# Kernel optimization log

Hardware: AMD Instinct MI355X
Metric: run time of the kernel (lower is better)

## Reference

```python
import jax, jax.numpy as jnp
import numpy as np

B, T, D = 4, 4096, 1024
P = 64  # d_model / n_head

def setup_inputs() -> dict:
    key = jax.random.key(0)
    k1, k2, k3 = jax.random.split(key, 3)
    x = jax.random.normal(k1, (B, T, D), dtype=jnp.float32)
    Wqkv = jax.random.normal(k2, (D, 3 * P), dtype=jnp.float32) * (1.0 / np.sqrt(D))
    bqkv = jax.random.normal(k3, (3 * P,), dtype=jnp.float32) * 0.01
    return {"x": x, "Wqkv": Wqkv, "bqkv": bqkv}

def reference(x, Wqkv, bqkv):
    Bv, Tv, Cv = x.shape
    qkv = (x @ Wqkv + bqkv).reshape(Bv, Tv, 3, P)  # [B,T,3,p]
    q, k, v = qkv[:, :, 0, :], qkv[:, :, 1, :], qkv[:, :, 2, :]
    # raw scores (source applies NO 1/sqrt(p) scaling)
    S = jnp.einsum('btp,bsp->bts', q, k)  # [B,T,T]
    causal = jnp.tril(jnp.ones((Tv, Tv), dtype=bool))
    S = jnp.where(causal[None, :, :], S, jnp.float32(-jnp.inf))
    Pm = jax.nn.softmax(S, axis=-1)
    O = jnp.einsum('bts,bsp->btp', Pm, v)  # [B,T,p]
    return O
```

## Files before the change

### kernel.cpp

```cpp
#include <hip/hip_runtime.h>
#include <hip/hip_fp16.h>

#define B_ 4
#define T_ 4096
#define D_ 1024
#define P_ 64

typedef _Float16 h8 __attribute__((ext_vector_type(8)));
typedef _Float16 h4 __attribute__((ext_vector_type(4)));
typedef float f32x4 __attribute__((ext_vector_type(4)));

__global__ __launch_bounds__(256) void wt_kernel(const float* __restrict__ W,
                                                 _Float16* __restrict__ Wt) {
    int idx = blockIdx.x * 256 + threadIdx.x;
    int n = idx >> 10, k = idx & 1023;
    Wt[idx] = (_Float16)W[k * 192 + n];
}

__global__ __launch_bounds__(256) void proj_kernel(
    const float* __restrict__ x, const _Float16* __restrict__ Wt,
    const float* __restrict__ bias,
    _Float16* __restrict__ qh, _Float16* __restrict__ kh, _Float16* __restrict__ vh)
{
    __shared__ _Float16 As[2][32][72];
    __shared__ _Float16 Bs[2][192][72];
    const int tid = threadIdx.x;
    const int w = tid >> 6, lane = tid & 63, quad = lane >> 4, l16 = lane & 15;
    const int row0 = blockIdx.x * 32;
    const int mstrip = w & 1;
    const int nbase = (w >> 1) * 6;

    float bvals[6];
#pragma unroll
    for (int nt = 0; nt < 6; nt++) bvals[nt] = bias[(nbase + nt) * 16 + l16];

    f32x4 acc[6];
#pragma unroll
    for (int i = 0; i < 6; i++) acc[i] = (f32x4){0.f, 0.f, 0.f, 0.f};

    const int arow = tid >> 3, ac0 = (tid & 7) * 8;

    float4 xa, xb;
    h8 wreg[6];
    {
        const float* xp = x + (size_t)(row0 + arow) * D_ + ac0;
        xa = *(const float4*)xp; xb = *(const float4*)(xp + 4);
#pragma unroll
        for (int p = 0; p < 6; p++) {
            int f = tid + 256 * p; int n = f >> 3, c0 = (f & 7) * 8;
            wreg[p] = *(const h8*)(Wt + (size_t)n * D_ + c0);
        }
    }

    for (int kc = 0; kc < 16; kc++) {
        const int buf = kc & 1;
        h8 av;
        av[0]=(_Float16)xa.x; av[1]=(_Float16)xa.y; av[2]=(_Float16)xa.z; av[3]=(_Float16)xa.w;
        av[4]=(_Float16)xb.x; av[5]=(_Float16)xb.y; av[6]=(_Float16)xb.z; av[7]=(_Float16)xb.w;
        *(h8*)&As[buf][arow][ac0] = av;
#pragma unroll
        for (int p = 0; p < 6; p++) {
            int f = tid + 256 * p; int n = f >> 3, c0 = (f & 7) * 8;
            *(h8*)&Bs[buf][n][c0] = wreg[p];
        }
        if (kc + 1 < 16) {
            int k0 = (kc + 1) * 64;
            const float* xp = x + (size_t)(row0 + arow) * D_ + k0 + ac0;
            xa = *(const float4*)xp; xb = *(const float4*)(xp + 4);
#pragma unroll
            for (int p = 0; p < 6; p++) {
                int f = tid + 256 * p; int n = f >> 3, c0 = (f & 7) * 8;
                wreg[p] = *(const h8*)(Wt + (size_t)n * D_ + k0 + c0);
            }
        }
        __syncthreads();
        h8 a0 = *(const h8*)&As[buf][16 * mstrip + l16][quad * 8];
        h8 a1 = *(const h8*)&As[buf][16 * mstrip + l16][32 + quad * 8];
#pragma unroll
        for (int nt = 0; nt < 6; nt++) {
            h8 b0 = *(const h8*)&Bs[buf][(nbase + nt) * 16 + l16][quad * 8];
            h8 b1 = *(const h8*)&Bs[buf][(nbase + nt) * 16 + l16][32 + quad * 8];
            acc[nt] = __builtin_amdgcn_mfma_f32_16x16x32_f16(a0, b0, acc[nt], 0, 0, 0);
            acc[nt] = __builtin_amdgcn_mfma_f32_16x16x32_f16(a1, b1, acc[nt], 0, 0, 0);
        }
    }

#pragma unroll
    for (int nt = 0; nt < 6; nt++) {
        int n = (nbase + nt) * 16 + l16;
        int g = n >> 6, p = n & 63;
        _Float16* dst = (g == 0) ? qh : (g == 1) ? kh : vh;
#pragma unroll
        for (int reg = 0; reg < 4; reg++) {
            int trow = row0 + 16 * mstrip + quad * 4 + reg;
            dst[(size_t)trow * 64 + p] = (_Float16)(acc[nt][reg] + bvals[nt]);
        }
    }
}

__global__ __launch_bounds__(256) void attn_kernel(
    const _Float16* __restrict__ qh, const _Float16* __restrict__ kh,
    const _Float16* __restrict__ vh, float* __restrict__ out,
    float* __restrict__ Opart, float2* __restrict__ ml,
    int lgC, int NC1, int direct)
{
    __shared__ _Float16 Vt[2][80][72];
    __shared__ _Float16 Ps[4][16][72];
    const int tid = threadIdx.x;
    const int w = tid >> 6, lane = tid & 63, quad = lane >> 4, l16 = lane & 15;
    const int C = 1 << lgC;

    const int cid = blockIdx.x;
    const int b = cid / NC1;
    int rem = cid - b * NC1;
    int qt = 0, k0 = 0, cnt = 1;
    for (int q = 0; q < 64; q++) {
        int nc = (q + C) >> lgC;
        if (rem < nc) { qt = q; k0 = rem << lgC; cnt = min(C, q + 1 - k0); break; }
        rem -= nc;
    }
    const size_t base = (size_t)b * T_ * 64;

#pragma unroll
    for (int buf = 0; buf < 2; buf++)
#pragma unroll
        for (int i = 0; i < 4; i++) {
            int r = 64 + i * 4 + w;
            Vt[buf][r][lane] = (r == 64) ? (_Float16)1.0f : (_Float16)0.0f;
        }

    h8 qf[2];
    {
        const _Float16* qp = qh + base + (size_t)(qt * 64 + 16 * w + l16) * 64 + quad * 8;
        qf[0] = *(const h8*)qp;
        qf[1] = *(const h8*)(qp + 32);
    }

    f32x4 o[5];
#pragma unroll
    for (int i = 0; i < 5; i++) o[i] = (f32x4){0.f, 0.f, 0.f, 0.f};
    float m[4];
#pragma unroll
    for (int r = 0; r < 4; r++) m[r] = -1e30f;

    const int vp0 = (tid & 15) * 4, vc0 = (tid >> 4) * 4;
    h4 vreg[4];
    {
        const _Float16* vp = vh + base + (size_t)(k0 * 64 + vc0) * 64 + vp0;
#pragma unroll
        for (int i = 0; i < 4; i++) vreg[i] = *(const h4*)(vp + (size_t)i * 64);
    }

    const int kend = k0 + cnt;
    for (int kt = k0; kt < kend; kt++) {
        const int bufi = kt & 1;
        h8 kf[4][2];
        {
            const _Float16* kp = kh + base + (size_t)(kt * 64 + l16) * 64 + quad * 8;
#pragma unroll
            for (int nt = 0; nt < 4; nt++) {
                kf[nt][0] = *(const h8*)(kp + (size_t)nt * 16 * 64);
                kf[nt][1] = *(const h8*)(kp + (size_t)nt * 16 * 64 + 32);
            }
        }
#pragma unroll
        for (int j = 0; j < 4; j++) {
            h4 t;
            t[0] = vreg[0][j]; t[1] = vreg[1][j]; t[2] = vreg[2][j]; t[3] = vreg[3][j];
            *(h4*)&Vt[bufi][vp0 + j][vc0] = t;
        }
        if (kt + 1 < kend) {
            const _Float16* vp = vh + base + (size_t)((kt + 1) * 64 + vc0) * 64 + vp0;
#pragma unroll
            for (int i = 0; i < 4; i++) vreg[i] = *(const h4*)(vp + (size_t)i * 64);
        }
        __syncthreads();

        f32x4 s[4];
#pragma unroll
        for (int nt = 0; nt < 4; nt++) {
            f32x4 c = (f32x4){0.f, 0.f, 0.f, 0.f};
            c = __builtin_amdgcn_mfma_f32_16x16x32_f16(qf[0], kf[nt][0], c, 0, 0, 0);
            c = __builtin_amdgcn_mfma_f32_16x16x32_f16(qf[1], kf[nt][1], c, 0, 0, 0);
            s[nt] = c;
        }

        if (kt == qt) {
#pragma unroll
            for (int nt = 0; nt < 4; nt++)
#pragma unroll
                for (int reg = 0; reg < 4; reg++) {
                    int col = nt * 16 + l16, row = 16 * w + quad * 4 + reg;
                    if (col > row) s[nt][reg] = -1e30f;
                }
        }

        float pexp[4][4];
#pragma unroll
        for (int reg = 0; reg < 4; reg++) {
            float mx = fmaxf(fmaxf(s[0][reg], s[1][reg]), fmaxf(s[2][reg], s[3][reg]));
            mx = fmaxf(mx, __shfl_xor(mx, 1));
            mx = fmaxf(mx, __shfl_xor(mx, 2));
            mx = fmaxf(mx, __shfl_xor(mx, 4));
            mx = fmaxf(mx, __shfl_xor(mx, 8));
            float mnew = fmaxf(m[reg], mx);
            float alpha = __expf(m[reg] - mnew);
            m[reg] = mnew;
#pragma unroll
            for (int nt = 0; nt < 4; nt++) pexp[nt][reg] = __expf(s[nt][reg] - mnew);
#pragma unroll
            for (int nt = 0; nt < 5; nt++) o[nt][reg] *= alpha;
        }

#pragma unroll
        for (int nt = 0; nt < 4; nt++)
#pragma unroll
            for (int reg = 0; reg < 4; reg++)
                Ps[w][quad * 4 + reg][nt * 16 + l16] = (_Float16)pexp[nt][reg];

#pragma unroll
        for (int kc = 0; kc < 2; kc++) {
            h8 pa = *(const h8*)&Ps[w][l16][kc * 32 + quad * 8];
#pragma unroll
            for (int nt = 0; nt < 5; nt++) {
                h8 vb = *(const h8*)&Vt[bufi][nt * 16 + l16][kc * 32 + quad * 8];
                o[nt] = __builtin_amdgcn_mfma_f32_16x16x32_f16(pa, vb, o[nt], 0, 0, 0);
            }
        }
    }

    if (direct) {
        float linv[4];
#pragma unroll
        for (int reg = 0; reg < 4; reg++) {
            float lv = __shfl(o[4][reg], quad << 4);
            linv[reg] = 1.0f / lv;
        }
#pragma unroll
        for (int nt = 0; nt < 4; nt++)
#pragma unroll
            for (int reg = 0; reg < 4; reg++) {
                int trow = qt * 64 + 16 * w + quad * 4 + reg;
                out[base + (size_t)trow * 64 + nt * 16 + l16] = o[nt][reg] * linv[reg];
            }
    } else {
        float* op = Opart + (size_t)cid * 4096;
#pragma unroll
        for (int nt = 0; nt < 4; nt++)
#pragma unroll
            for (int reg = 0; reg < 4; reg++)
                op[(16 * w + quad * 4 + reg) * 64 + nt * 16 + l16] = o[nt][reg];
        if (l16 == 0) {
#pragma unroll
            for (int reg = 0; reg < 4; reg++) {
                int r = 16 * w + quad * 4 + reg;
                ml[(size_t)cid * 64 + r] = make_float2(m[reg], o[4][reg]);
            }
        }
    }
}

__global__ __launch_bounds__(256) void combine_kernel(
    const float* __restrict__ Opart, const float2* __restrict__ ml,
    float* __restrict__ out, int lgC, int NC1)
{
    const int C = 1 << lgC;
    const int task = blockIdx.x;
    const int b = task >> 6, qt = task & 63;
    int pref = 0;
    for (int q = 0; q < qt; q++) pref += (q + C) >> lgC;
    const int cbase = b * NC1 + pref;
    const int nch = (qt + C) >> lgC;

    const int r = threadIdx.x >> 2;
    const int c0 = (threadIdx.x & 3) << 4;

    float M = -1e30f;
    for (int i = 0; i < nch; i++) M = fmaxf(M, ml[(size_t)(cbase + i) * 64 + r].x);
    float L = 0.f, acc[16];
#pragma unroll
    for (int t = 0; t < 16; t++) acc[t] = 0.f;
    for (int i = 0; i < nch; i++) {
        float2 v = ml[(size_t)(cbase + i) * 64 + r];
        float sc = __expf(v.x - M);
        L += sc * v.y;
        const float* op = Opart + (size_t)(cbase + i) * 4096 + r * 64 + c0;
#pragma unroll
        for (int t = 0; t < 4; t++) {
            float4 x4 = *(const float4*)(op + 4 * t);
            acc[4*t+0] += sc * x4.x; acc[4*t+1] += sc * x4.y;
            acc[4*t+2] += sc * x4.z; acc[4*t+3] += sc * x4.w;
        }
    }
    float inv = 1.0f / L;
    float* po = out + ((size_t)b * T_ + qt * 64 + r) * 64 + c0;
#pragma unroll
    for (int t = 0; t < 4; t++) {
        float4 x4 = { acc[4*t]*inv, acc[4*t+1]*inv, acc[4*t+2]*inv, acc[4*t+3]*inv };
        *(float4*)(po + 4 * t) = x4;
    }
}

extern "C" void kernel_launch(void* const* d_in, const int* in_sizes, int n_in,
                              void* d_out, int out_size, void* d_ws, size_t ws_size,
                              hipStream_t stream) {
    const float* x    = (const float*)d_in[0];
    const float* W    = (const float*)d_in[1];
    const float* bias = (const float*)d_in[2];
    float* out = (float*)d_out;
    char* ws = (char*)d_ws;
    _Float16* qh = (_Float16*)(ws);
    _Float16* kh = (_Float16*)(ws + (size_t)2 * 1024 * 1024);
    _Float16* vh = (_Float16*)(ws + (size_t)4 * 1024 * 1024);
    _Float16* Wt = (_Float16*)(ws + (size_t)6 * 1024 * 1024);
    const size_t pbase = (size_t)8 * 1024 * 1024;

    int lgC = -1, nc1 = 64;
    for (int lg = 3; lg <= 6; lg++) {
        int C = 1 << lg, n1 = 0;
        for (int q = 0; q < 64; q++) n1 += (q + C) >> lg;
        size_t need = pbase + (size_t)4 * n1 * (4096 * 4 + 64 * 8);
        if (need <= ws_size) { lgC = lg; nc1 = n1; break; }
    }
    int direct = (lgC < 0) ? 1 : 0;
    if (direct) { lgC = 6; nc1 = 64; }
    float*  Opart = (float*)(ws + pbase);
    float2* mlp   = (float2*)(ws + pbase + (size_t)4 * nc1 * 4096 * 4);

    wt_kernel<<<768, 256, 0, stream>>>(W, Wt);
    proj_kernel<<<512, 256, 0, stream>>>(x, Wt, bias, qh, kh, vh);
    attn_kernel<<<4 * nc1, 256, 0, stream>>>(qh, kh, vh, out, Opart, mlp, lgC, nc1, direct);
    if (!direct)
        combine_kernel<<<256, 256, 0, stream>>>(Opart, mlp, out, lgC, nc1);
}
```

Baseline: 175.7 us.

## Rework attention to 128-row query tiles with LDS-staged K and exp2 softmax

Each attention block now covers 128 query rows, with 32 rows per wave. K tiles are staged through double-buffered LDS. Scores are computed transposed, so P stays in registers and feeds the PV MFMAs directly with no LDS round trip. Q is prescaled by log2e so the softmax can use exp2, and the row sum l is tracked explicitly instead of through an augmented ones column in V. Partial outputs are stored in fp16, the chunk size search now starts lower, and the W transpose and projection kernels are retiled (the projection splits N across two blocks). Together these aim to cut LDS traffic and redundant K loads. The cost is more registers per thread, occupancy now set through launch bounds, and slightly lower precision in the partial outputs.

New measurement: 176.2 us. No clear change (+0.3%).

```diff
diff --git a/kernel.cpp b/kernel.cpp
--- a/kernel.cpp
+++ b/kernel.cpp
@@ -4,17 +4,37 @@
 #define B_ 4
 #define T_ 4096
 #define D_ 1024
-#define P_ 64
 
 typedef _Float16 h8 __attribute__((ext_vector_type(8)));
 typedef _Float16 h4 __attribute__((ext_vector_type(4)));
 typedef float f32x4 __attribute__((ext_vector_type(4)));
 
+#define LOG2E 1.44269504088896340736f
+#define MASKV -3.0e38f
+#define MINIT -1.0e30f
+#define EXP2(x) __builtin_amdgcn_exp2f(x)
+
 __global__ __launch_bounds__(256) void wt_kernel(const float* __restrict__ W,
                                                  _Float16* __restrict__ Wt) {
-    int idx = blockIdx.x * 256 + threadIdx.x;
-    int n = idx >> 10, k = idx & 1023;
-    Wt[idx] = (_Float16)W[k * 192 + n];
+    __shared__ _Float16 Tr[192][20];
+    const int tid = threadIdx.x, k0 = blockIdx.x * 16;
+#pragma unroll
+    for (int i = 0; i < 3; i++) {
+        int fi = tid + 256 * i;
+        int r = fi / 48, c4 = fi % 48;
+        float4 v = *(const float4*)(W + (size_t)(k0 + r) * 192 + c4 * 4);
+        Tr[c4 * 4 + 0][r] = (_Float16)v.x;
+        Tr[c4 * 4 + 1][r] = (_Float16)v.y;
+        Tr[c4 * 4 + 2][r] = (_Float16)v.z;
+        Tr[c4 * 4 + 3][r] = (_Float16)v.w;
+    }
+    __syncthreads();
+#pragma unroll
+    for (int i = 0; i < 3; i++) {
+        int oi = tid + 256 * i;
+        int n = oi >> 2, kq = oi & 3;
+        *(h4*)(Wt + (size_t)n * D_ + k0 + kq * 4) = *(const h4*)&Tr[n][kq * 4];
+    }
 }
 
 __global__ __launch_bounds__(256) void proj_kernel(
@@ -23,32 +43,33 @@
     _Float16* __restrict__ qh, _Float16* __restrict__ kh, _Float16* __restrict__ vh)
 {
     __shared__ _Float16 As[2][32][72];
-    __shared__ _Float16 Bs[2][192][72];
+    __shared__ _Float16 Bs[2][96][72];
     const int tid = threadIdx.x;
     const int w = tid >> 6, lane = tid & 63, quad = lane >> 4, l16 = lane & 15;
-    const int row0 = blockIdx.x * 32;
+    const int row0 = (blockIdx.x >> 1) * 32;
+    const int nb0 = (blockIdx.x & 1) * 96;
     const int mstrip = w & 1;
-    const int nbase = (w >> 1) * 6;
-
-    float bvals[6];
-#pragma unroll
-    for (int nt = 0; nt < 6; nt++) bvals[nt] = bias[(nbase + nt) * 16 + l16];
-
-    f32x4 acc[6];
-#pragma unroll
-    for (int i = 0; i < 6; i++) acc[i] = (f32x4){0.f, 0.f, 0.f, 0.f};
+    const int ngrp = (w >> 1) * 3;
+
+    float bvals[3];
+#pragma unroll
+    for (int nt = 0; nt < 3; nt++) bvals[nt] = bias[nb0 + (ngrp + nt) * 16 + l16];
+
+    f32x4 acc[3];
+#pragma unroll
+    for (int i = 0; i < 3; i++) acc[i] = (f32x4){0.f, 0.f, 0.f, 0.f};
 
     const int arow = tid >> 3, ac0 = (tid & 7) * 8;
 
     float4 xa, xb;
-    h8 wreg[6];
+    h8 wreg[3];
     {
         const float* xp = x + (size_t)(row0 + arow) * D_ + ac0;
         xa = *(const float4*)xp; xb = *(const float4*)(xp + 4);
 #pragma unroll
-        for (int p = 0; p < 6; p++) {
+        for (int p = 0; p < 3; p++) {
             int f = tid + 256 * p; int n = f >> 3, c0 = (f & 7) * 8;
-            wreg[p] = *(const h8*)(Wt + (size_t)n * D_ + c0);
+            wreg[p] = *(const h8*)(Wt + (size_t)(nb0 + n) * D_ + c0);
         }
     }
 
@@ -59,7 +80,7 @@
         av[4]=(_Float16)xb.x; av[5]=(_Float16)xb.y; av[6]=(_Float16)xb.z; av[7]=(_Float16)xb.w;
         *(h8*)&As[buf][arow][ac0] = av;
 #pragma unroll
-        for (int p = 0; p < 6; p++) {
+        for (int p = 0; p < 3; p++) {
             int f = tid + 256 * p; int n = f >> 3, c0 = (f & 7) * 8;
             *(h8*)&Bs[buf][n][c0] = wreg[p];
         }
@@ -68,44 +89,45 @@
             const float* xp = x + (size_t)(row0 + arow) * D_ + k0 + ac0;
             xa = *(const float4*)xp; xb = *(const float4*)(xp + 4);
 #pragma unroll
-            for (int p = 0; p < 6; p++) {
+            for (int p = 0; p < 3; p++) {
                 int f = tid + 256 * p; int n = f >> 3, c0 = (f & 7) * 8;
-                wreg[p] = *(const h8*)(Wt + (size_t)n * D_ + k0 + c0);
+                wreg[p] = *(const h8*)(Wt + (size_t)(nb0 + n) * D_ + k0 + c0);
             }
         }
         __syncthreads();
         h8 a0 = *(const h8*)&As[buf][16 * mstrip + l16][quad * 8];
         h8 a1 = *(const h8*)&As[buf][16 * mstrip + l16][32 + quad * 8];
 #pragma unroll
-        for (int nt = 0; nt < 6; nt++) {
-            h8 b0 = *(const h8*)&Bs[buf][(nbase + nt) * 16 + l16][quad * 8];
-            h8 b1 = *(const h8*)&Bs[buf][(nbase + nt) * 16 + l16][32 + quad * 8];
+        for (int nt = 0; nt < 3; nt++) {
+            h8 b0 = *(const h8*)&Bs[buf][(ngrp + nt) * 16 + l16][quad * 8];
+            h8 b1 = *(const h8*)&Bs[buf][(ngrp + nt) * 16 + l16][32 + quad * 8];
             acc[nt] = __builtin_amdgcn_mfma_f32_16x16x32_f16(a0, b0, acc[nt], 0, 0, 0);
             acc[nt] = __builtin_amdgcn_mfma_f32_16x16x32_f16(a1, b1, acc[nt], 0, 0, 0);
         }
     }
 
 #pragma unroll
-    for (int nt = 0; nt < 6; nt++) {
-        int n = (nbase + nt) * 16 + l16;
+    for (int nt = 0; nt < 3; nt++) {
+        int n = nb0 + (ngrp + nt) * 16 + l16;
         int g = n >> 6, p = n & 63;
         _Float16* dst = (g == 0) ? qh : (g == 1) ? kh : vh;
+        float scale = (g == 0) ? LOG2E : 1.0f;
 #pragma unroll
         for (int reg = 0; reg < 4; reg++) {
             int trow = row0 + 16 * mstrip + quad * 4 + reg;
-            dst[(size_t)trow * 64 + p] = (_Float16)(acc[nt][reg] + bvals[nt]);
-        }
-    }
-}
-
-__global__ __launch_bounds__(256) void attn_kernel(
+            dst[(size_t)trow * 64 + p] = (_Float16)((acc[nt][reg] + bvals[nt]) * scale);
+        }
+    }
+}
+
+__global__ __launch_bounds__(256, 4) void attn_kernel(
     const _Float16* __restrict__ qh, const _Float16* __restrict__ kh,
     const _Float16* __restrict__ vh, float* __restrict__ out,
-    float* __restrict__ Opart, float2* __restrict__ ml,
+    _Float16* __restrict__ Opart, float2* __restrict__ ml,
     int lgC, int NC1, int direct)
 {
-    __shared__ _Float16 Vt[2][80][72];
-    __shared__ _Float16 Ps[4][16][72];
+    __shared__ _Float16 Ks[2][64][72];
+    __shared__ _Float16 Vt[2][64][72];
     const int tid = threadIdx.x;
     const int w = tid >> 6, lane = tid & 63, quad = lane >> 4, l16 = lane & 15;
     const int C = 1 << lgC;
@@ -113,39 +135,36 @@
     const int cid = blockIdx.x;
     const int b = cid / NC1;
     int rem = cid - b * NC1;
-    int qt = 0, k0 = 0, cnt = 1;
-    for (int q = 0; q < 64; q++) {
-        int nc = (q + C) >> lgC;
-        if (rem < nc) { qt = q; k0 = rem << lgC; cnt = min(C, q + 1 - k0); break; }
+    int qt2 = 0, k0 = 0, cnt = 1;
+    for (int i = 0; i < 32; i++) {
+        int nc = (2 * i + 2 + C - 1) >> lgC;
+        if (rem < nc) { qt2 = i; k0 = rem << lgC; cnt = min(C, 2 * i + 2 - k0); break; }
         rem -= nc;
     }
     const size_t base = (size_t)b * T_ * 64;
-
-#pragma unroll
-    for (int buf = 0; buf < 2; buf++)
-#pragma unroll
-        for (int i = 0; i < 4; i++) {
-            int r = 64 + i * 4 + w;
-            Vt[buf][r][lane] = (r == 64) ? (_Float16)1.0f : (_Float16)0.0f;
-        }
-
-    h8 qf[2];
-    {
-        const _Float16* qp = qh + base + (size_t)(qt * 64 + 16 * w + l16) * 64 + quad * 8;
-        qf[0] = *(const h8*)qp;
-        qf[1] = *(const h8*)(qp + 32);
-    }
-
-    f32x4 o[5];
-#pragma unroll
-    for (int i = 0; i < 5; i++) o[i] = (f32x4){0.f, 0.f, 0.f, 0.f};
-    float m[4];
-#pragma unroll
-    for (int r = 0; r < 4; r++) m[r] = -1e30f;
-
+    const int qbase = qt2 * 128 + w * 32;
+
+    h8 qf[2][2];
+#pragma unroll
+    for (int u = 0; u < 2; u++) {
+        const _Float16* qp = qh + base + (size_t)(qbase + u * 16 + l16) * 64 + quad * 8;
+        qf[u][0] = *(const h8*)qp;
+        qf[u][1] = *(const h8*)(qp + 32);
+    }
+
+    f32x4 o[8];
+#pragma unroll
+    for (int i = 0; i < 8; i++) o[i] = (f32x4){0.f, 0.f, 0.f, 0.f};
+    float m[2] = {MINIT, MINIT}, l[2] = {0.f, 0.f};
+
+    const int krow = tid >> 3, kc0 = (tid & 7) * 8;
     const int vp0 = (tid & 15) * 4, vc0 = (tid >> 4) * 4;
+    h8 kreg[2];
     h4 vreg[4];
     {
+        const _Float16* kp = kh + base + (size_t)(k0 * 64) * 64;
+        kreg[0] = *(const h8*)(kp + (size_t)krow * 64 + kc0);
+        kreg[1] = *(const h8*)(kp + (size_t)(krow + 32) * 64 + kc0);
         const _Float16* vp = vh + base + (size_t)(k0 * 64 + vc0) * 64 + vp0;
 #pragma unroll
         for (int i = 0; i < 4; i++) vreg[i] = *(const h4*)(vp + (size_t)i * 64);
@@ -153,152 +172,156 @@
 
     const int kend = k0 + cnt;
     for (int kt = k0; kt < kend; kt++) {
-        const int bufi = kt & 1;
-        h8 kf[4][2];
-        {
-            const _Float16* kp = kh + base + (size_t)(kt * 64 + l16) * 64 + quad * 8;
-#pragma unroll
-            for (int nt = 0; nt < 4; nt++) {
-                kf[nt][0] = *(const h8*)(kp + (size_t)nt * 16 * 64);
-                kf[nt][1] = *(const h8*)(kp + (size_t)nt * 16 * 64 + 32);
-            }
-        }
+        const int buf = kt & 1;
+        *(h8*)&Ks[buf][krow][kc0] = kreg[0];
+        *(h8*)&Ks[buf][krow + 32][kc0] = kreg[1];
 #pragma unroll
         for (int j = 0; j < 4; j++) {
             h4 t;
             t[0] = vreg[0][j]; t[1] = vreg[1][j]; t[2] = vreg[2][j]; t[3] = vreg[3][j];
-            *(h4*)&Vt[bufi][vp0 + j][vc0] = t;
+            *(h4*)&Vt[buf][vp0 + j][vc0] = t;
         }
         if (kt + 1 < kend) {
+            const _Float16* kp = kh + base + (size_t)((kt + 1) * 64) * 64;
+            kreg[0] = *(const h8*)(kp + (size_t)krow * 64 + kc0);
+            kreg[1] = *(const h8*)(kp + (size_t)(krow + 32) * 64 + kc0);
             const _Float16* vp = vh + base + (size_t)((kt + 1) * 64 + vc0) * 64 + vp0;
 #pragma unroll
             for (int i = 0; i < 4; i++) vreg[i] = *(const h4*)(vp + (size_t)i * 64);
         }
         __syncthreads();
 
-        f32x4 s[4];
-#pragma unroll
-        for (int nt = 0; nt < 4; nt++) {
-            f32x4 c = (f32x4){0.f, 0.f, 0.f, 0.f};
-            c = __builtin_amdgcn_mfma_f32_16x16x32_f16(qf[0], kf[nt][0], c, 0, 0, 0);
-            c = __builtin_amdgcn_mfma_f32_16x16x32_f16(qf[1], kf[nt][1], c, 0, 0, 0);
-            s[nt] = c;
-        }
-
-        if (kt == qt) {
-#pragma unroll
-            for (int nt = 0; nt < 4; nt++)
-#pragma unroll
-                for (int reg = 0; reg < 4; reg++) {
-                    int col = nt * 16 + l16, row = 16 * w + quad * 4 + reg;
-                    if (col > row) s[nt][reg] = -1e30f;
+        const bool skip = (kt * 64) > (qbase + 31);
+        if (!skip) {
+            f32x4 s[2][4];
+#pragma unroll
+            for (int nt = 0; nt < 4; nt++) {
+                h8 kf0 = *(const h8*)&Ks[buf][nt * 16 + l16][quad * 8];
+                h8 kf1 = *(const h8*)&Ks[buf][nt * 16 + l16][32 + quad * 8];
+#pragma unroll
+                for (int u = 0; u < 2; u++) {
+                    f32x4 c = (f32x4){0.f, 0.f, 0.f, 0.f};
+                    c = __builtin_amdgcn_mfma_f32_16x16x32_f16(kf0, qf[u][0], c, 0, 0, 0);
+                    c = __builtin_amdgcn_mfma_f32_16x16x32_f16(kf1, qf[u][1], c, 0, 0, 0);
+                    s[u][nt] = c;
                 }
-        }
-
-        float pexp[4][4];
-#pragma unroll
-        for (int reg = 0; reg < 4; reg++) {
-            float mx = fmaxf(fmaxf(s[0][reg], s[1][reg]), fmaxf(s[2][reg], s[3][reg]));
-            mx = fmaxf(mx, __shfl_xor(mx, 1));
-            mx = fmaxf(mx, __shfl_xor(mx, 2));
-            mx = fmaxf(mx, __shfl_xor(mx, 4));
-            mx = fmaxf(mx, __shfl_xor(mx, 8));
-            float mnew = fmaxf(m[reg], mx);
-            float alpha = __expf(m[reg] - mnew);
-            m[reg] = mnew;
-#pragma unroll
-            for (int nt = 0; nt < 4; nt++) pexp[nt][reg] = __expf(s[nt][reg] - mnew);
-#pragma unroll
-            for (int nt = 0; nt < 5; nt++) o[nt][reg] *= alpha;
-        }
-
-#pragma unroll
-        for (int nt = 0; nt < 4; nt++)
-#pragma unroll
-            for (int reg = 0; reg < 4; reg++)
-                Ps[w][quad * 4 + reg][nt * 16 + l16] = (_Float16)pexp[nt][reg];
-
-#pragma unroll
-        for (int kc = 0; kc < 2; kc++) {
-            h8 pa = *(const h8*)&Ps[w][l16][kc * 32 + quad * 8];
-#pragma unroll
-            for (int nt = 0; nt < 5; nt++) {
-                h8 vb = *(const h8*)&Vt[bufi][nt * 16 + l16][kc * 32 + quad * 8];
-                o[nt] = __builtin_amdgcn_mfma_f32_16x16x32_f16(pa, vb, o[nt], 0, 0, 0);
             }
+
+            h4 pf[2][4];
+#pragma unroll
+            for (int u = 0; u < 2; u++) {
+                const int qrow = qbase + u * 16 + l16;
+                if (kt * 64 + 63 > qbase + u * 16) {
+#pragma unroll
+                    for (int nt = 0; nt < 4; nt++)
+#pragma unroll
+                        for (int reg = 0; reg < 4; reg++) {
+                            int sg = kt * 64 + nt * 16 + quad * 4 + reg;
+                            if (sg > qrow) s[u][nt][reg] = MASKV;
+                        }
+                }
+                float mx = s[u][0][0];
+#pragma unroll
+                for (int nt = 0; nt < 4; nt++)
+#pragma unroll
+                    for (int reg = 0; reg < 4; reg++) mx = fmaxf(mx, s[u][nt][reg]);
+                mx = fmaxf(mx, __shfl_xor(mx, 16));
+                mx = fmaxf(mx, __shfl_xor(mx, 32));
+                float mnew = fmaxf(m[u], mx);
+                float alpha = EXP2(m[u] - mnew);
+                m[u] = mnew;
+                float rs = 0.f;
+#pragma unroll
+                for (int nt = 0; nt < 4; nt++) {
+#pragma unroll
+                    for (int reg = 0; reg < 4; reg++) {
+                        float p = EXP2(s[u][nt][reg] - mnew);
+                        s[u][nt][reg] = p;
+                        rs += p;
+                    }
+                    h4 ph;
+                    ph[0]=(_Float16)s[u][nt][0]; ph[1]=(_Float16)s[u][nt][1];
+                    ph[2]=(_Float16)s[u][nt][2]; ph[3]=(_Float16)s[u][nt][3];
+                    pf[u][nt] = ph;
+                }
+                rs += __shfl_xor(rs, 16);
+                rs += __shfl_xor(rs, 32);
+                l[u] = l[u] * alpha + rs;
+#pragma unroll
+                for (int pt = 0; pt < 4; pt++)
+#pragma unroll
+                    for (int reg = 0; reg < 4; reg++) o[u * 4 + pt][reg] *= alpha;
+            }
+
+#pragma unroll
+            for (int pt = 0; pt < 4; pt++)
+#pragma unroll
+                for (int nt = 0; nt < 4; nt++) {
+                    h4 vf = *(const h4*)&Vt[buf][pt * 16 + l16][nt * 16 + quad * 4];
+                    o[pt]     = __builtin_amdgcn_mfma_f32_16x16x16f16(vf, pf[0][nt], o[pt], 0, 0, 0);
+                    o[4 + pt] = __builtin_amdgcn_mfma_f32_16x16x16f16(vf, pf[1][nt], o[4 + pt], 0, 0, 0);
+                }
         }
     }
 
     if (direct) {
-        float linv[4];
-#pragma unroll
-        for (int reg = 0; reg < 4; reg++) {
-            float lv = __shfl(o[4][reg], quad << 4);
-            linv[reg] = 1.0f / lv;
-        }
-#pragma unroll
-        for (int nt = 0; nt < 4; nt++)
-#pragma unroll
-            for (int reg = 0; reg < 4; reg++) {
-                int trow = qt * 64 + 16 * w + quad * 4 + reg;
-                out[base + (size_t)trow * 64 + nt * 16 + l16] = o[nt][reg] * linv[reg];
+#pragma unroll
+        for (int u = 0; u < 2; u++) {
+            float linv = 1.0f / l[u];
+            int trow = qt2 * 128 + w * 32 + u * 16 + l16;
+#pragma unroll
+            for (int pt = 0; pt < 4; pt++)
+#pragma unroll
+                for (int reg = 0; reg < 4; reg++)
+                    out[base + (size_t)trow * 64 + pt * 16 + quad * 4 + reg] =
+                        o[u * 4 + pt][reg] * linv;
+        }
+    } else {
+        _Float16* op = Opart + (size_t)cid * 8192;
+#pragma unroll
+        for (int u = 0; u < 2; u++) {
+            int r = w * 32 + u * 16 + l16;
+#pragma unroll
+            for (int pt = 0; pt < 4; pt++) {
+                h4 ph;
+#pragma unroll
+                for (int reg = 0; reg < 4; reg++) ph[reg] = (_Float16)o[u * 4 + pt][reg];
+                *(h4*)(op + (size_t)r * 64 + pt * 16 + quad * 4) = ph;
             }
-    } else {
-        float* op = Opart + (size_t)cid * 4096;
-#pragma unroll
-        for (int nt = 0; nt < 4; nt++)
-#pragma unroll
-            for (int reg = 0; reg < 4; reg++)
-                op[(16 * w + quad * 4 + reg) * 64 + nt * 16 + l16] = o[nt][reg];
-        if (l16 == 0) {
-#pragma unroll
-            for (int reg = 0; reg < 4; reg++) {
-                int r = 16 * w + quad * 4 + reg;
-                ml[(size_t)cid * 64 + r] = make_float2(m[reg], o[4][reg]);
-            }
+            if (quad == 0) ml[(size_t)cid * 128 + r] = make_float2(m[u], l[u]);
         }
     }
 }
 
 __global__ __launch_bounds__(256) void combine_kernel(
-    const float* __restrict__ Opart, const float2* __restrict__ ml,
+    const _Float16* __restrict__ Opart, const float2* __restrict__ ml,
     float* __restrict__ out, int lgC, int NC1)
 {
     const int C = 1 << lgC;
     const int task = blockIdx.x;
-    const int b = task >> 6, qt = task & 63;
+    const int b = task >> 8, tile = (task >> 3) & 31, rg = task & 7;
     int pref = 0;
-    for (int q = 0; q < qt; q++) pref += (q + C) >> lgC;
+    for (int i = 0; i < tile; i++) pref += (2 * i + 2 + C - 1) >> lgC;
     const int cbase = b * NC1 + pref;
-    const int nch = (qt + C) >> lgC;
-
-    const int r = threadIdx.x >> 2;
-    const int c0 = (threadIdx.x & 3) << 4;
-
-    float M = -1e30f;
-    for (int i = 0; i < nch; i++) M = fmaxf(M, ml[(size_t)(cbase + i) * 64 + r].x);
-    float L = 0.f, acc[16];
-#pragma unroll
-    for (int t = 0; t < 16; t++) acc[t] = 0.f;
+    const int nch = (2 * tile + 2 + C - 1) >> lgC;
+
+    const int r = rg * 16 + (threadIdx.x >> 4);
+    const int c0 = (threadIdx.x & 15) * 4;
+
+    float M = MINIT;
+    for (int i = 0; i < nch; i++) M = fmaxf(M, ml[(size_t)(cbase + i) * 128 + r].x);
+    float L = 0.f, acc[4] = {0.f, 0.f, 0.f, 0.f};
     for (int i = 0; i < nch; i++) {
-        float2 v = ml[(size_t)(cbase + i) * 64 + r];
-        float sc = __expf(v.x - M);
+        float2 v = ml[(size_t)(cbase + i) * 128 + r];
+        float sc = EXP2(v.x - M);
         L += sc * v.y;
-        const float* op = Opart + (size_t)(cbase + i) * 4096 + r * 64 + c0;
-#pragma unroll
-        for (int t = 0; t < 4; t++) {
-            float4 x4 = *(const float4*)(op + 4 * t);
-            acc[4*t+0] += sc * x4.x; acc[4*t+1] += sc * x4.y;
-            acc[4*t+2] += sc * x4.z; acc[4*t+3] += sc * x4.w;
-        }
+        h4 x4 = *(const h4*)(Opart + (size_t)(cbase + i) * 8192 + (size_t)r * 64 + c0);
+#pragma unroll
+        for (int t = 0; t < 4; t++) acc[t] += sc * (float)x4[t];
     }
     float inv = 1.0f / L;
-    float* po = out + ((size_t)b * T_ + qt * 64 + r) * 64 + c0;
-#pragma unroll
-    for (int t = 0; t < 4; t++) {
-        float4 x4 = { acc[4*t]*inv, acc[4*t+1]*inv, acc[4*t+2]*inv, acc[4*t+3]*inv };
-        *(float4*)(po + 4 * t) = x4;
-    }
+    float4 res = { acc[0]*inv, acc[1]*inv, acc[2]*inv, acc[3]*inv };
+    *(float4*)(out + ((size_t)b * T_ + tile * 128 + r) * 64 + c0) = res;
 }
 
 extern "C" void kernel_launch(void* const* d_in, const int* in_sizes, int n_in,
@@ -315,21 +338,21 @@
     _Float16* Wt = (_Float16*)(ws + (size_t)6 * 1024 * 1024);
     const size_t pbase = (size_t)8 * 1024 * 1024;
 
-    int lgC = -1, nc1 = 64;
-    for (int lg = 3; lg <= 6; lg++) {
+    int lgC = -1, nc1 = 32;
+    for (int lg = 2; lg <= 6; lg++) {
         int C = 1 << lg, n1 = 0;
-        for (int q = 0; q < 64; q++) n1 += (q + C) >> lg;
-        size_t need = pbase + (size_t)4 * n1 * (4096 * 4 + 64 * 8);
+        for (int i = 0; i < 32; i++) n1 += (2 * i + 2 + C - 1) >> lg;
+        size_t need = pbase + (size_t)4 * n1 * (8192 * 2 + 128 * 8);
         if (need <= ws_size) { lgC = lg; nc1 = n1; break; }
     }
     int direct = (lgC < 0) ? 1 : 0;
-    if (direct) { lgC = 6; nc1 = 64; }
-    float*  Opart = (float*)(ws + pbase);
-    float2* mlp   = (float2*)(ws + pbase + (size_t)4 * nc1 * 4096 * 4);
-
-    wt_kernel<<<768, 256, 0, stream>>>(W, Wt);
-    proj_kernel<<<512, 256, 0, stream>>>(x, Wt, bias, qh, kh, vh);
+    if (direct) { lgC = 6; nc1 = 32; }
+    _Float16* Opart = (_Float16*)(ws + pbase);
+    float2*   mlp   = (float2*)(ws + pbase + (size_t)4 * nc1 * 8192 * 2);
+
+    wt_kernel<<<64, 256, 0, stream>>>(W, Wt);
+    proj_kernel<<<1024, 256, 0, stream>>>(x, Wt, bias, qh, kh, vh);
     attn_kernel<<<4 * nc1, 256, 0, stream>>>(qh, kh, vh, out, Opart, mlp, lgC, nc1, direct);
     if (!direct)
-        combine_kernel<<<256, 256, 0, stream>>>(Opart, mlp, out, lgC, nc1);
-}
+        combine_kernel<<<1024, 256, 0, stream>>>(Opart, mlp, out, lgC, nc1);
+}
```
